# Optimization experiments

Measured on AMD Instinct MI355X. Metric: run time of the kernel, lower is better.

The kernel has to match this reference:

```python
import jax, jax.numpy as jnp
import numpy as np

N_NODES = 50000
N_EDGES = 400000
HIDDEN = 128
OUT_DIM = 1
N_LAYERS = 3
NUM_GRAPHS = 64
VOCAB = 101


def _lin(x, w, b):
    return x @ w + b


def setup_inputs() -> dict:
    key = jax.random.key(0)
    ks = jax.random.split(key, 20)
    inp = {}
    inp['z'] = jax.random.randint(ks[0], (N_NODES,), 0, VOCAB)
    inp['edge_index'] = jax.random.randint(ks[1], (2, N_EDGES), 0, N_NODES)
    inp['edge_attr'] = jax.random.normal(ks[2], (N_EDGES, 1), dtype=jnp.float32)
    inp['batch'] = jnp.sort(jax.random.randint(ks[3], (N_NODES,), 0, NUM_GRAPHS))
    s = 0.05
    inp['embed'] = jax.random.normal(ks[4], (VOCAB, HIDDEN), dtype=jnp.float32) * s
    # per-layer stacked params; weights stored [in, out]
    inp['msg_w1'] = jax.random.normal(ks[5], (N_LAYERS, 2 * HIDDEN + 1, HIDDEN), dtype=jnp.float32) * s
    inp['msg_b1'] = jnp.zeros((N_LAYERS, HIDDEN), dtype=jnp.float32)
    inp['msg_w2'] = jax.random.normal(ks[6], (N_LAYERS, HIDDEN, HIDDEN), dtype=jnp.float32) * s
    inp['msg_b2'] = jnp.zeros((N_LAYERS, HIDDEN), dtype=jnp.float32)
    inp['upd_w1'] = jax.random.normal(ks[7], (N_LAYERS, 2 * HIDDEN, HIDDEN), dtype=jnp.float32) * s
    inp['upd_b1'] = jnp.zeros((N_LAYERS, HIDDEN), dtype=jnp.float32)
    inp['upd_w2'] = jax.random.normal(ks[8], (N_LAYERS, HIDDEN, HIDDEN), dtype=jnp.float32) * s
    inp['upd_b2'] = jnp.zeros((N_LAYERS, HIDDEN), dtype=jnp.float32)
    inp['head_w1'] = jax.random.normal(ks[9], (HIDDEN, HIDDEN), dtype=jnp.float32) * s
    inp['head_b1'] = jnp.zeros((HIDDEN,), dtype=jnp.float32)
    inp['head_w2'] = jax.random.normal(ks[10], (HIDDEN, OUT_DIM), dtype=jnp.float32) * s
    inp['head_b2'] = jnp.zeros((OUT_DIM,), dtype=jnp.float32)
    return inp


def reference(z, edge_index, edge_attr, batch, embed, msg_w1, msg_b1, msg_w2, msg_b2,
              upd_w1, upd_b1, upd_w2, upd_b2, head_w1, head_b1, head_w2, head_b2):
    src, dst = edge_index[0], edge_index[1]
    h = embed[z]  # [N, H]
    for l in range(N_LAYERS):
        m_in = jnp.concatenate([h[src], h[dst], edge_attr], axis=1)  # [E, 2H+1]
        msg = _lin(jax.nn.relu(_lin(m_in, msg_w1[l], msg_b1[l])), msg_w2[l], msg_b2[l])
        agg = jax.ops.segment_sum(msg, dst, num_segments=N_NODES)  # [N, H]
        upd_in = jnp.concatenate([h, agg], axis=1)  # [N, 2H]
        h = h + _lin(jax.nn.relu(_lin(upd_in, upd_w1[l], upd_b1[l])), upd_w2[l], upd_b2[l])
    pooled = jax.ops.segment_sum(h, batch, num_segments=NUM_GRAPHS)
    counts = jax.ops.segment_sum(jnp.ones((h.shape[0], 1), h.dtype), batch, num_segments=NUM_GRAPHS)
    pooled = pooled / jnp.maximum(counts, 1.0)
    return _lin(jax.nn.relu(_lin(pooled, head_w1, head_b1)), head_w2, head_b2)
```

## Files before the change

### kernel.cpp

```cpp
#include <hip/hip_runtime.h>

#define N_NODES 50000
#define NPAD 50048
#define N_EDGES 400000
#define HID 128
#define NUM_GRAPHS 64
#define SCAN_B 196
#define ECAP 2048

typedef __bf16 bf16;
typedef bf16 bf16x8 __attribute__((ext_vector_type(8)));
typedef float f32x4 __attribute__((ext_vector_type(4)));

__device__ inline bf16x8 cvt8(const float* p) {
    const float4 a = *(const float4*)p;
    const float4 b = *(const float4*)(p + 4);
    bf16x8 v;
    v[0] = (bf16)a.x; v[1] = (bf16)a.y; v[2] = (bf16)a.z; v[3] = (bf16)a.w;
    v[4] = (bf16)b.x; v[5] = (bf16)b.y; v[6] = (bf16)b.z; v[7] = (bf16)b.w;
    return v;
}

__device__ __forceinline__ void tile_out(const bf16* lds, bf16* g, int n0, int tid) {
    #pragma unroll
    for (int u = 0; u < 4; ++u) {
        const int unit = u * 256 + tid;
        const int row = unit >> 4;
        const int ci = (unit & 15) * 8;
        *(bf16x8*)&g[(size_t)(n0 + row) * HID + ci] =
            *(const bf16x8*)&lds[row * 136 + ci];
    }
}

__global__ void k_hist(const int* __restrict__ edst, int* __restrict__ deg) {
    int e = blockIdx.x * 256 + threadIdx.x;
    if (e < N_EDGES) atomicAdd(&deg[edst[e]], 1);
}

__global__ void k_scan1(const int* __restrict__ deg, int* __restrict__ partial) {
    __shared__ int buf[256];
    int i = blockIdx.x * 256 + threadIdx.x;
    buf[threadIdx.x] = (i < N_NODES) ? deg[i] : 0;
    __syncthreads();
    for (int off = 128; off > 0; off >>= 1) {
        if (threadIdx.x < off) buf[threadIdx.x] += buf[threadIdx.x + off];
        __syncthreads();
    }
    if (threadIdx.x == 0) partial[blockIdx.x] = buf[0];
}

__global__ void k_scan2(int* __restrict__ partial, int* __restrict__ row_ptr) {
    __shared__ int buf[256];
    int v = (threadIdx.x < SCAN_B) ? partial[threadIdx.x] : 0;
    buf[threadIdx.x] = v;
    __syncthreads();
    for (int off = 1; off < 256; off <<= 1) {
        int t = (threadIdx.x >= off) ? buf[threadIdx.x - off] : 0;
        __syncthreads();
        buf[threadIdx.x] += t;
        __syncthreads();
    }
    if (threadIdx.x < SCAN_B) partial[threadIdx.x] = buf[threadIdx.x] - v;
    if (threadIdx.x == 255) row_ptr[N_NODES] = buf[255];
}

__global__ void k_scan3(const int* __restrict__ deg, const int* __restrict__ partial,
                        int* __restrict__ row_ptr, int* __restrict__ cursor) {
    __shared__ int buf[256];
    int i = blockIdx.x * 256 + threadIdx.x;
    int v = (i < N_NODES) ? deg[i] : 0;
    buf[threadIdx.x] = v;
    __syncthreads();
    for (int off = 1; off < 256; off <<= 1) {
        int t = (threadIdx.x >= off) ? buf[threadIdx.x - off] : 0;
        __syncthreads();
        buf[threadIdx.x] += t;
        __syncthreads();
    }
    if (i < N_NODES) {
        int ex = partial[blockIdx.x] + buf[threadIdx.x] - v;
        row_ptr[i] = ex;
        cursor[i] = ex;
    }
}

__global__ void k_scatter(const int* __restrict__ esrc, const int* __restrict__ edst,
                          const float* __restrict__ attr, int* __restrict__ cursor,
                          int* __restrict__ s_src, float* __restrict__ s_attr) {
    int e = blockIdx.x * 256 + threadIdx.x;
    if (e >= N_EDGES) return;
    int p = atomicAdd(&cursor[edst[e]], 1);
    s_src[p] = esrc[e];
    s_attr[p] = attr[e];
}

__global__ void k_wprep(const float* __restrict__ msg_w1, const float* __restrict__ upd_w1,
                        const float* __restrict__ upd_w2,
                        bf16* __restrict__ W1t, bf16* __restrict__ U1t,
                        bf16* __restrict__ U2t) {
    const int l = blockIdx.y;
    const int n = blockIdx.x, k = threadIdx.x;
    const float* w1  = msg_w1 + (size_t)l * 257 * HID;
    const float* uw1 = upd_w1 + (size_t)l * 2 * HID * HID;
    const float* uw2 = upd_w2 + (size_t)l * HID * HID;
    if (n < 256) {
        W1t[(size_t)l * 256 * HID + n * HID + k] =
            (bf16)w1[(size_t)((n & 128) + k) * HID + (n & 127)];
    } else if (n < 384) {
        const int nn = n - 256;
        U1t[(size_t)l * HID * HID + nn * HID + k] = (bf16)uw1[(size_t)k * HID + nn];
    } else {
        const int nn = n - 384;
        U2t[(size_t)l * HID * HID + nn * HID + k] = (bf16)uw2[(size_t)k * HID + nn];
    }
}

__global__ void k_small(const float* __restrict__ msg_w2, const float* __restrict__ upd_w1,
                        const float* __restrict__ msg_b2,
                        bf16* __restrict__ W2Ut, float* __restrict__ b2u) {
    __shared__ float row[HID];
    const int l = blockIdx.y;
    const int k = blockIdx.x, j = threadIdx.x;
    const float* w2  = msg_w2 + (size_t)l * HID * HID;
    const float* uw1 = upd_w1 + (size_t)l * 2 * HID * HID;
    const float* b2  = msg_b2 + (size_t)l * HID;
    const float* src = (k < HID) ? &w2[(size_t)k * HID] : b2;
    row[j] = src[j];
    __syncthreads();
    float acc = 0.f;
    #pragma unroll 8
    for (int m = 0; m < HID; ++m)
        acc = fmaf(row[m], uw1[(size_t)(HID + m) * HID + j], acc);
    if (k < HID) W2Ut[(size_t)l * HID * HID + (size_t)j * HID + k] = (bf16)acc;
    else b2u[l * HID + j] = acc;
}

__launch_bounds__(256, 4)
__global__ void k_embed_pre(const int* __restrict__ z, const float* __restrict__ embed,
                            const bf16* __restrict__ W1t, const float* __restrict__ b1,
                            bf16* __restrict__ h16, bf16* __restrict__ P, bf16* __restrict__ Q) {
    __shared__ bf16 sH[64 * 136];
    __shared__ bf16 sH2[64 * 136];
    const int tid = threadIdx.x;
    const int n0 = blockIdx.x * 64;
    {
        const int r = tid & 63, cg = tid >> 6;
        const int n = n0 + r;
        const bool valid = n < N_NODES;
        const float* src = valid ? &embed[(size_t)z[n] * HID + cg * 32] : embed;
        #pragma unroll
        for (int i = 0; i < 4; ++i) {
            bf16x8 v;
            if (valid) {
                v = cvt8(src + i * 8);
            } else {
                for (int j = 0; j < 8; ++j) v[j] = (bf16)0.f;
            }
            *(bf16x8*)&sH[r * 136 + cg * 32 + i * 8] = v;
        }
    }
    __syncthreads();
    tile_out(sH, h16, n0, tid);

    const int lane = tid & 63, wave = tid >> 6;
    const int lr = lane & 15, kq = (lane >> 4) * 8, rq = (lane >> 4) * 4;
    const int bcol = wave * 64;

    const f32x4 z4 = {0.f, 0.f, 0.f, 0.f};
    f32x4 acc[4][4];
    #pragma unroll
    for (int mi = 0; mi < 4; ++mi)
        #pragma unroll
        for (int ni = 0; ni < 4; ++ni) acc[mi][ni] = z4;

    #pragma unroll
    for (int ks = 0; ks < 4; ++ks) {
        bf16x8 av[4], bv[4];
        #pragma unroll
        for (int mi = 0; mi < 4; ++mi)
            av[mi] = *(const bf16x8*)&sH[(mi * 16 + lr) * 136 + ks * 32 + kq];
        #pragma unroll
        for (int ni = 0; ni < 4; ++ni)
            bv[ni] = *(const bf16x8*)&W1t[(size_t)(bcol + ni * 16 + lr) * HID + ks * 32 + kq];
        #pragma unroll
        for (int mi = 0; mi < 4; ++mi)
            #pragma unroll
            for (int ni = 0; ni < 4; ++ni)
                acc[mi][ni] = __builtin_amdgcn_mfma_f32_16x16x32_bf16(av[mi], bv[ni],
                                                                      acc[mi][ni], 0, 0, 0);
    }
    __syncthreads();

    {
        bf16* sOut = (bcol < 128) ? sH : sH2;
        const int cb = bcol & 127;
        #pragma unroll
        for (int ni = 0; ni < 4; ++ni) {
            const int c = cb + ni * 16 + lr;
            const float bias = (bcol >= 128) ? b1[c] : 0.f;
            #pragma unroll
            for (int mi = 0; mi < 4; ++mi)
                #pragma unroll
                for (int r = 0; r < 4; ++r)
                    sOut[(mi * 16 + rq + r) * 136 + c] = (bf16)(acc[mi][ni][r] + bias);
        }
    }
    __syncthreads();
    tile_out(sH, P, n0, tid);
    tile_out(sH2, Q, n0, tid);
}

template<int DO_PRE>
__launch_bounds__(256, 4)
__global__ void k_layer(bf16* __restrict__ h16,
                        const bf16* __restrict__ P, const bf16* __restrict__ Q,
                        const int* __restrict__ row_ptr, const int* __restrict__ s_src,
                        const float* __restrict__ s_attr, const float* __restrict__ w1last,
                        const bf16* __restrict__ U1t, const bf16* __restrict__ W2Ut,
                        const float* __restrict__ ub1, const float* __restrict__ b2u,
                        const bf16* __restrict__ U2t, const float* __restrict__ ub2,
                        const bf16* __restrict__ W1tn, const float* __restrict__ b1n,
                        bf16* __restrict__ Pn, bf16* __restrict__ Qn,
                        const int* __restrict__ batch, float* __restrict__ pooled) {
    __shared__ bf16 sAgg[64 * 136];
    __shared__ bf16 sT[64 * 136];
    __shared__ float sDeg[64];
    const int tid = threadIdx.x;
    const int n0 = blockIdx.x * 64;

    {
        int*   sEsrc = (int*)sT;
        float* sEatt = (float*)(sT + ECAP * 2);
        const int elo = row_ptr[n0];
        const int ehi = row_ptr[min(n0 + 64, N_NODES)];
        const int ecap = min(ehi - elo, ECAP);
        for (int i = tid; i < ecap; i += 256) {
            sEsrc[i] = s_src[elo + i];
            sEatt[i] = s_attr[elo + i];
        }
        __syncthreads();

        const int grp = tid >> 4, ln = tid & 15, c8 = ln * 8;
        float wl[8];
        #pragma unroll
        for (int j = 0; j < 8; ++j) wl[j] = w1last[c8 + j];
        #pragma unroll
        for (int t = 0; t < 4; ++t) {
            const int row = t * 16 + grp;
            const int n = n0 + row;
            float a8[8];
            #pragma unroll
            for (int j = 0; j < 8; ++j) a8[j] = 0.f;
            if (n < N_NODES) {
                const int lo = row_ptr[n], hi = row_ptr[n + 1];
                if (ln == 0) sDeg[row] = (float)(hi - lo);
                const bf16x8 qv = *(const bf16x8*)&Q[(size_t)n * HID + c8];
                float q8[8];
                #pragma unroll
                for (int j = 0; j < 8; ++j) q8[j] = (float)qv[j];
                const int llo = lo - elo, lhi = hi - elo;
                if (lhi <= ecap) {
                    int e = llo;
                    for (; e + 4 <= lhi; e += 4) {
                        const int s0 = sEsrc[e], s1 = sEsrc[e + 1];
                        const int s2 = sEsrc[e + 2], s3 = sEsrc[e + 3];
                        const float t0 = sEatt[e], t1 = sEatt[e + 1];
                        const float t2 = sEatt[e + 2], t3 = sEatt[e + 3];
                        const bf16x8 p0 = *(const bf16x8*)&P[(size_t)s0 * HID + c8];
                        const bf16x8 p1 = *(const bf16x8*)&P[(size_t)s1 * HID + c8];
                        const bf16x8 p2 = *(const bf16x8*)&P[(size_t)s2 * HID + c8];
                        const bf16x8 p3 = *(const bf16x8*)&P[(size_t)s3 * HID + c8];
                        #pragma unroll
                        for (int j = 0; j < 8; ++j) {
                            a8[j] += fmaxf(fmaf(t0, wl[j], q8[j] + (float)p0[j]), 0.f);
                            a8[j] += fmaxf(fmaf(t1, wl[j], q8[j] + (float)p1[j]), 0.f);
                            a8[j] += fmaxf(fmaf(t2, wl[j], q8[j] + (float)p2[j]), 0.f);
                            a8[j] += fmaxf(fmaf(t3, wl[j], q8[j] + (float)p3[j]), 0.f);
                        }
                    }
                    for (; e < lhi; ++e) {
                        const int s0 = sEsrc[e];
                        const float t0 = sEatt[e];
                        const bf16x8 p0 = *(const bf16x8*)&P[(size_t)s0 * HID + c8];
                        #pragma unroll
                        for (int j = 0; j < 8; ++j)
                            a8[j] += fmaxf(fmaf(t0, wl[j], q8[j] + (float)p0[j]), 0.f);
                    }
                } else {
                    for (int e = lo; e < hi; ++e) {
                        const int s0 = s_src[e];
                        const float t0 = s_attr[e];
                        const bf16x8 p0 = *(const bf16x8*)&P[(size_t)s0 * HID + c8];
                        #pragma unroll
                        for (int j = 0; j < 8; ++j)
                            a8[j] += fmaxf(fmaf(t0, wl[j], q8[j] + (float)p0[j]), 0.f);
                    }
                }
            } else if (ln == 0) {
                sDeg[row] = 0.f;
            }
            bf16x8 o;
            #pragma unroll
            for (int j = 0; j < 8; ++j) o[j] = (bf16)a8[j];
            *(bf16x8*)&sAgg[row * 136 + c8] = o;
        }
    }
    __syncthreads();

    const int lane = tid & 63, wave = tid >> 6;
    const int lr = lane & 15, kq = (lane >> 4) * 8, rq = (lane >> 4) * 4;
    const int nw = wave * 32;
    const f32x4 z4 = {0.f, 0.f, 0.f, 0.f};

    f32x4 acc[4][2];
    #pragma unroll
    for (int mi = 0; mi < 4; ++mi) { acc[mi][0] = z4; acc[mi][1] = z4; }

    #pragma unroll
    for (int ks = 0; ks < 4; ++ks) {
        bf16x8 av[4], bv[2];
        #pragma unroll
        for (int mi = 0; mi < 4; ++mi)
            av[mi] = *(const bf16x8*)&h16[(size_t)(n0 + mi * 16 + lr) * HID + ks * 32 + kq];
        #pragma unroll
        for (int ni = 0; ni < 2; ++ni)
            bv[ni] = *(const bf16x8*)&U1t[(size_t)(nw + ni * 16 + lr) * HID + ks * 32 + kq];
        #pragma unroll
        for (int mi = 0; mi < 4; ++mi)
            #pragma unroll
            for (int ni = 0; ni < 2; ++ni)
                acc[mi][ni] = __builtin_amdgcn_mfma_f32_16x16x32_bf16(av[mi], bv[ni],
                                                                      acc[mi][ni], 0, 0, 0);
    }
    #pragma unroll
    for (int ks = 0; ks < 4; ++ks) {
        bf16x8 av[4], bv[2];
        #pragma unroll
        for (int mi = 0; mi < 4; ++mi)
            av[mi] = *(const bf16x8*)&sAgg[(mi * 16 + lr) * 136 + ks * 32 + kq];
        #pragma unroll
        for (int ni = 0; ni < 2; ++ni)
            bv[ni] = *(const bf16x8*)&W2Ut[(size_t)(nw + ni * 16 + lr) * HID + ks * 32 + kq];
        #pragma unroll
        for (int mi = 0; mi < 4; ++mi)
            #pragma unroll
            for (int ni = 0; ni < 2; ++ni)
                acc[mi][ni] = __builtin_amdgcn_mfma_f32_16x16x32_bf16(av[mi], bv[ni],
                                                                      acc[mi][ni], 0, 0, 0);
    }
    __syncthreads();

    #pragma unroll
    for (int ni = 0; ni < 2; ++ni) {
        const int c = nw + ni * 16 + lr;
        const float bb1 = ub1[c], bb2 = b2u[c];
        #pragma unroll
        for (int mi = 0; mi < 4; ++mi)
            #pragma unroll
            for (int r = 0; r < 4; ++r) {
                const int row = mi * 16 + rq + r;
                float v = acc[mi][ni][r] + bb1 + sDeg[row] * bb2;
                sT[row * 136 + c] = (bf16)fmaxf(v, 0.f);
            }
    }
    __syncthreads();

    f32x4 acc2[4][2];
    #pragma unroll
    for (int mi = 0; mi < 4; ++mi) { acc2[mi][0] = z4; acc2[mi][1] = z4; }
    #pragma unroll
    for (int ks = 0; ks < 4; ++ks) {
        bf16x8 av[4], bv[2];
        #pragma unroll
        for (int mi = 0; mi < 4; ++mi)
            av[mi] = *(const bf16x8*)&sT[(mi * 16 + lr) * 136 + ks * 32 + kq];
        #pragma unroll
        for (int ni = 0; ni < 2; ++ni)
            bv[ni] = *(const bf16x8*)&U2t[(size_t)(nw + ni * 16 + lr) * HID + ks * 32 + kq];
        #pragma unroll
        for (int mi = 0; mi < 4; ++mi)
            #pragma unroll
            for (int ni = 0; ni < 2; ++ni)
                acc2[mi][ni] = __builtin_amdgcn_mfma_f32_16x16x32_bf16(av[mi], bv[ni],
                                                                       acc2[mi][ni], 0, 0, 0);
    }
    __syncthreads();

    #pragma unroll
    for (int ni = 0; ni < 2; ++ni) {
        const int c = nw + ni * 16 + lr;
        const float bb = ub2[c];
        #pragma unroll
        for (int mi = 0; mi < 4; ++mi)
            #pragma unroll
            for (int r = 0; r < 4; ++r) {
                const int row = mi * 16 + rq + r;
                const int gr = n0 + row;
                float nh = 0.f;
                if (gr < N_NODES) {
                    const size_t off = (size_t)gr * HID + c;
                    nh = (float)h16[off] + acc2[mi][ni][r] + bb;
                }
                sT[row * 136 + c] = (bf16)nh;
                if (DO_PRE) sAgg[row * 136 + c] = (bf16)nh;
            }
    }
    __syncthreads();

    if (DO_PRE) {
        tile_out(sT, h16, n0, tid);

        const int bcol = wave * 64;
        f32x4 pacc[4][4];
        #pragma unroll
        for (int mi = 0; mi < 4; ++mi)
            #pragma unroll
            for (int ni = 0; ni < 4; ++ni) pacc[mi][ni] = z4;

        #pragma unroll
        for (int ks = 0; ks < 4; ++ks) {
            bf16x8 av[4], bv[4];
            #pragma unroll
            for (int mi = 0; mi < 4; ++mi)
                av[mi] = *(const bf16x8*)&sAgg[(mi * 16 + lr) * 136 + ks * 32 + kq];
            #pragma unroll
            for (int ni = 0; ni < 4; ++ni)
                bv[ni] = *(const bf16x8*)&W1tn[(size_t)(bcol + ni * 16 + lr) * HID + ks * 32 + kq];
            #pragma unroll
            for (int mi = 0; mi < 4; ++mi)
                #pragma unroll
                for (int ni = 0; ni < 4; ++ni)
                    pacc[mi][ni] = __builtin_amdgcn_mfma_f32_16x16x32_bf16(av[mi], bv[ni],
                                                                           pacc[mi][ni], 0, 0, 0);
        }
        __syncthreads();

        {
            bf16* sOut = (bcol < 128) ? sT : sAgg;
            const int cb = bcol & 127;
            #pragma unroll
            for (int ni = 0; ni < 4; ++ni) {
                const int c = cb + ni * 16 + lr;
                const float bias = (bcol >= 128) ? b1n[c] : 0.f;
                #pragma unroll
                for (int mi = 0; mi < 4; ++mi)
                    #pragma unroll
                    for (int r = 0; r < 4; ++r)
                        sOut[(mi * 16 + rq + r) * 136 + c] = (bf16)(pacc[mi][ni][r] + bias);
            }
        }
        __syncthreads();
        tile_out(sT, Pn, n0, tid);
        tile_out(sAgg, Qn, n0, tid);
    } else {
        const int c = tid & 127;
        const int half = tid >> 7;
        const int rows = min(64, N_NODES - n0);
        const int rbeg = half * 32;
        const int rend = min(rbeg + 32, rows);
        int cur = -1;
        float s = 0.f;
        for (int r = rbeg; r < rend; ++r) {
            const int g = batch[n0 + r];
            const float v = (float)sT[r * 136 + c];
            if (g != cur) {
                if (cur >= 0) atomicAdd(&pooled[cur * HID + c], s);
                cur = g; s = v;
            } else {
                s += v;
            }
        }
        if (cur >= 0) atomicAdd(&pooled[cur * HID + c], s);
    }
}

__device__ inline int lb(const int* a, int n, int v) {
    int lo = 0, hi = n;
    while (lo < hi) { int m = (lo + hi) >> 1; if (a[m] < v) lo = m + 1; else hi = m; }
    return lo;
}

__global__ void k_head(const float* __restrict__ pooled, const int* __restrict__ batch,
                       const float* __restrict__ hw1, const float* __restrict__ hb1,
                       const float* __restrict__ hw2, const float* __restrict__ hb2,
                       float* __restrict__ out) {
    const int g = blockIdx.x;
    const int c = threadIdx.x;
    __shared__ float sp[HID];
    __shared__ float red[HID];
    __shared__ int sb[2];
    if (c == 0) { sb[0] = lb(batch, N_NODES, g); sb[1] = lb(batch, N_NODES, g + 1); }
    __syncthreads();
    const float cnt = fmaxf((float)(sb[1] - sb[0]), 1.f);
    sp[c] = pooled[g * HID + c] / cnt;
    __syncthreads();
    float acc = hb1[c];
    #pragma unroll 8
    for (int k = 0; k < HID; ++k) acc = fmaf(sp[k], hw1[k * HID + c], acc);
    red[c] = fmaxf(acc, 0.f) * hw2[c];
    __syncthreads();
    for (int s = 64; s > 0; s >>= 1) {
        if (c < s) red[c] += red[c + s];
        __syncthreads();
    }
    if (c == 0) out[g] = red[0] + hb2[0];
}

extern "C" void kernel_launch(void* const* d_in, const int* in_sizes, int n_in,
                              void* d_out, int out_size, void* d_ws, size_t ws_size,
                              hipStream_t stream) {
    const int*   z       = (const int*)d_in[0];
    const int*   ei      = (const int*)d_in[1];
    const float* eattr   = (const float*)d_in[2];
    const int*   batch   = (const int*)d_in[3];
    const float* embed   = (const float*)d_in[4];
    const float* msg_w1  = (const float*)d_in[5];
    const float* msg_b1  = (const float*)d_in[6];
    const float* msg_w2  = (const float*)d_in[7];
    const float* msg_b2  = (const float*)d_in[8];
    const float* upd_w1  = (const float*)d_in[9];
    const float* upd_b1  = (const float*)d_in[10];
    const float* upd_w2  = (const float*)d_in[11];
    const float* upd_b2  = (const float*)d_in[12];
    const float* head_w1 = (const float*)d_in[13];
    const float* head_b1 = (const float*)d_in[14];
    const float* head_w2 = (const float*)d_in[15];
    const float* head_b2 = (const float*)d_in[16];
    float* out = (float*)d_out;

    float* pooled = (float*)d_ws;
    float* b2u    = pooled + NUM_GRAPHS * HID;
    float* s_attr = b2u + 3 * HID;
    int* deg_i    = (int*)(s_attr + N_EDGES);
    int* row_ptr  = deg_i + N_NODES;
    int* partial  = row_ptr + N_NODES + 1;
    int* cursor   = partial + 256;
    int* s_src    = cursor + N_NODES;
    bf16* h16     = (bf16*)((((unsigned long long)(s_src + N_EDGES)) + 15ULL) & ~15ULL);
    bf16* P0      = h16 + (size_t)NPAD * HID;
    bf16* Q0      = P0 + (size_t)NPAD * HID;
    bf16* P1      = Q0 + (size_t)NPAD * HID;
    bf16* Q1      = P1 + (size_t)NPAD * HID;
    bf16* W1t     = Q1 + (size_t)NPAD * HID;
    bf16* U1t     = W1t + 3 * 256 * HID;
    bf16* W2Ut    = U1t + 3 * HID * HID;
    bf16* U2t     = W2Ut + 3 * HID * HID;

    const int* esrc = ei;
    const int* edst = ei + N_EDGES;

    hipMemsetAsync(deg_i, 0, N_NODES * sizeof(int), stream);
    hipMemsetAsync(pooled, 0, NUM_GRAPHS * HID * sizeof(float), stream);
    k_hist<<<(N_EDGES + 255) / 256, 256, 0, stream>>>(edst, deg_i);
    k_scan1<<<SCAN_B, 256, 0, stream>>>(deg_i, partial);
    k_scan2<<<1, 256, 0, stream>>>(partial, row_ptr);
    k_scan3<<<SCAN_B, 256, 0, stream>>>(deg_i, partial, row_ptr, cursor);
    k_scatter<<<(N_EDGES + 255) / 256, 256, 0, stream>>>(esrc, edst, eattr, cursor, s_src, s_attr);
    {
        dim3 g1(512, 3);
        k_wprep<<<g1, 128, 0, stream>>>(msg_w1, upd_w1, upd_w2, W1t, U1t, U2t);
        dim3 g2(HID + 1, 3);
        k_small<<<g2, HID, 0, stream>>>(msg_w2, upd_w1, msg_b2, W2Ut, b2u);
    }

    const int nblk = NPAD / 64;
    k_embed_pre<<<nblk, 256, 0, stream>>>(z, embed, W1t, msg_b1, h16, P0, Q0);

    bf16* Pa = P0; bf16* Qa = Q0; bf16* Pb = P1; bf16* Qb = Q1;
    for (int l = 0; l < 3; ++l) {
        const float* w1last = msg_w1 + (size_t)l * 257 * HID + 256 * HID;
        const bf16* U1l  = U1t  + (size_t)l * HID * HID;
        const bf16* W2Ul = W2Ut + (size_t)l * HID * HID;
        const bf16* U2l  = U2t  + (size_t)l * HID * HID;
        if (l < 2) {
            k_layer<1><<<nblk, 256, 0, stream>>>(
                h16, Pa, Qa, row_ptr, s_src, s_attr, w1last,
                U1l, W2Ul, upd_b1 + (size_t)l * HID, b2u + l * HID,
                U2l, upd_b2 + (size_t)l * HID,
                W1t + (size_t)(l + 1) * 256 * HID, msg_b1 + (size_t)(l + 1) * HID, Pb, Qb,
                nullptr, nullptr);
            bf16* tp = Pa; Pa = Pb; Pb = tp;
            bf16* tq = Qa; Qa = Qb; Qb = tq;
        } else {
            k_layer<0><<<nblk, 256, 0, stream>>>(
                h16, Pa, Qa, row_ptr, s_src, s_attr, w1last,
                U1l, W2Ul, upd_b1 + (size_t)l * HID, b2u + l * HID,
                U2l, upd_b2 + (size_t)l * HID,
                nullptr, nullptr, nullptr, nullptr,
                batch, pooled);
        }
    }
    k_head<<<NUM_GRAPHS, 128, 0, stream>>>(pooled, batch, head_w1, head_b1, head_w2, head_b2, out);
}
```

Before: 277.2 us.

## Split edge aggregation out of fused layer kernel into separate high-occupancy kernel

Moves the per-node gather-and-ReLU edge aggregation out of the fused layer kernel into its own kernel, k_agg. k_agg has a smaller LDS footprint and launch bounds that allow more waves per CU, which should hide the latency of the irregular gathers better. The aggregated result now makes a round trip through a global bf16 buffer, adding an extra write and read of N×128 per layer plus an extra launch. The layer kernel reads the aggregate straight from global memory into its MFMA operands and gets node degrees from a small shared copy of row_ptr.

```diff
diff --git a/kernel.cpp b/kernel.cpp
--- a/kernel.cpp
+++ b/kernel.cpp
@@ -6,7 +6,7 @@
 #define HID 128
 #define NUM_GRAPHS 64
 #define SCAN_B 196
-#define ECAP 2048
+#define EC 1024
 
 typedef __bf16 bf16;
 typedef bf16 bf16x8 __attribute__((ext_vector_type(8)));
@@ -210,102 +210,105 @@
     tile_out(sH2, Q, n0, tid);
 }
 
+__launch_bounds__(256, 6)
+__global__ void k_agg(const bf16* __restrict__ P, const bf16* __restrict__ Q,
+                      const int* __restrict__ row_ptr, const int* __restrict__ s_src,
+                      const float* __restrict__ s_attr, const float* __restrict__ w1last,
+                      bf16* __restrict__ aggH) {
+    __shared__ int   sEsrc[EC];
+    __shared__ float sEatt[EC];
+    const int tid = threadIdx.x;
+    const int n0 = blockIdx.x * 64;
+    const int elo = row_ptr[n0];
+    const int ehi = row_ptr[min(n0 + 64, N_NODES)];
+    const int ecap = min(ehi - elo, EC);
+    for (int i = tid; i < ecap; i += 256) {
+        sEsrc[i] = s_src[elo + i];
+        sEatt[i] = s_attr[elo + i];
+    }
+    __syncthreads();
+
+    const int grp = tid >> 4, ln = tid & 15, c8 = ln * 8;
+    float wl[8];
+    #pragma unroll
+    for (int j = 0; j < 8; ++j) wl[j] = w1last[c8 + j];
+    #pragma unroll
+    for (int t = 0; t < 4; ++t) {
+        const int n = n0 + t * 16 + grp;
+        if (n >= N_NODES) continue;
+        float a8[8];
+        #pragma unroll
+        for (int j = 0; j < 8; ++j) a8[j] = 0.f;
+        const int lo = row_ptr[n], hi = row_ptr[n + 1];
+        const bf16x8 qv = *(const bf16x8*)&Q[(size_t)n * HID + c8];
+        float q8[8];
+        #pragma unroll
+        for (int j = 0; j < 8; ++j) q8[j] = (float)qv[j];
+        const int llo = lo - elo, lhi = hi - elo;
+        if (lhi <= ecap) {
+            int e = llo;
+            for (; e + 4 <= lhi; e += 4) {
+                const int s0 = sEsrc[e], s1 = sEsrc[e + 1];
+                const int s2 = sEsrc[e + 2], s3 = sEsrc[e + 3];
+                const float t0 = sEatt[e], t1 = sEatt[e + 1];
+                const float t2 = sEatt[e + 2], t3 = sEatt[e + 3];
+                const bf16x8 p0 = *(const bf16x8*)&P[(size_t)s0 * HID + c8];
+                const bf16x8 p1 = *(const bf16x8*)&P[(size_t)s1 * HID + c8];
+                const bf16x8 p2 = *(const bf16x8*)&P[(size_t)s2 * HID + c8];
+                const bf16x8 p3 = *(const bf16x8*)&P[(size_t)s3 * HID + c8];
+                #pragma unroll
+                for (int j = 0; j < 8; ++j) {
+                    a8[j] += fmaxf(fmaf(t0, wl[j], q8[j] + (float)p0[j]), 0.f);
+                    a8[j] += fmaxf(fmaf(t1, wl[j], q8[j] + (float)p1[j]), 0.f);
+                    a8[j] += fmaxf(fmaf(t2, wl[j], q8[j] + (float)p2[j]), 0.f);
+                    a8[j] += fmaxf(fmaf(t3, wl[j], q8[j] + (float)p3[j]), 0.f);
+                }
+            }
+            for (; e < lhi; ++e) {
+                const int s0 = sEsrc[e];
+                const float t0 = sEatt[e];
+                const bf16x8 p0 = *(const bf16x8*)&P[(size_t)s0 * HID + c8];
+                #pragma unroll
+                for (int j = 0; j < 8; ++j)
+                    a8[j] += fmaxf(fmaf(t0, wl[j], q8[j] + (float)p0[j]), 0.f);
+            }
+        } else {
+            for (int e = lo; e < hi; ++e) {
+                const int s0 = s_src[e];
+                const float t0 = s_attr[e];
+                const bf16x8 p0 = *(const bf16x8*)&P[(size_t)s0 * HID + c8];
+                #pragma unroll
+                for (int j = 0; j < 8; ++j)
+                    a8[j] += fmaxf(fmaf(t0, wl[j], q8[j] + (float)p0[j]), 0.f);
+            }
+        }
+        bf16x8 o;
+        #pragma unroll
+        for (int j = 0; j < 8; ++j) o[j] = (bf16)a8[j];
+        *(bf16x8*)&aggH[(size_t)n * HID + c8] = o;
+    }
+}
+
 template<int DO_PRE>
 __launch_bounds__(256, 4)
-__global__ void k_layer(bf16* __restrict__ h16,
-                        const bf16* __restrict__ P, const bf16* __restrict__ Q,
-                        const int* __restrict__ row_ptr, const int* __restrict__ s_src,
-                        const float* __restrict__ s_attr, const float* __restrict__ w1last,
+__global__ void k_layer(bf16* __restrict__ h16, const bf16* __restrict__ aggH,
+                        const int* __restrict__ row_ptr,
                         const bf16* __restrict__ U1t, const bf16* __restrict__ W2Ut,
                         const float* __restrict__ ub1, const float* __restrict__ b2u,
                         const bf16* __restrict__ U2t, const float* __restrict__ ub2,
                         const bf16* __restrict__ W1tn, const float* __restrict__ b1n,
                         bf16* __restrict__ Pn, bf16* __restrict__ Qn,
                         const int* __restrict__ batch, float* __restrict__ pooled) {
-    __shared__ bf16 sAgg[64 * 136];
+    __shared__ bf16 sP[64 * 136];
     __shared__ bf16 sT[64 * 136];
     __shared__ float sDeg[64];
+    __shared__ int sRP[65];
     const int tid = threadIdx.x;
     const int n0 = blockIdx.x * 64;
 
-    {
-        int*   sEsrc = (int*)sT;
-        float* sEatt = (float*)(sT + ECAP * 2);
-        const int elo = row_ptr[n0];
-        const int ehi = row_ptr[min(n0 + 64, N_NODES)];
-        const int ecap = min(ehi - elo, ECAP);
-        for (int i = tid; i < ecap; i += 256) {
-            sEsrc[i] = s_src[elo + i];
-            sEatt[i] = s_attr[elo + i];
-        }
-        __syncthreads();
-
-        const int grp = tid >> 4, ln = tid & 15, c8 = ln * 8;
-        float wl[8];
-        #pragma unroll
-        for (int j = 0; j < 8; ++j) wl[j] = w1last[c8 + j];
-        #pragma unroll
-        for (int t = 0; t < 4; ++t) {
-            const int row = t * 16 + grp;
-            const int n = n0 + row;
-            float a8[8];
-            #pragma unroll
-            for (int j = 0; j < 8; ++j) a8[j] = 0.f;
-            if (n < N_NODES) {
-                const int lo = row_ptr[n], hi = row_ptr[n + 1];
-                if (ln == 0) sDeg[row] = (float)(hi - lo);
-                const bf16x8 qv = *(const bf16x8*)&Q[(size_t)n * HID + c8];
-                float q8[8];
-                #pragma unroll
-                for (int j = 0; j < 8; ++j) q8[j] = (float)qv[j];
-                const int llo = lo - elo, lhi = hi - elo;
-                if (lhi <= ecap) {
-                    int e = llo;
-                    for (; e + 4 <= lhi; e += 4) {
-                        const int s0 = sEsrc[e], s1 = sEsrc[e + 1];
-                        const int s2 = sEsrc[e + 2], s3 = sEsrc[e + 3];
-                        const float t0 = sEatt[e], t1 = sEatt[e + 1];
-                        const float t2 = sEatt[e + 2], t3 = sEatt[e + 3];
-                        const bf16x8 p0 = *(const bf16x8*)&P[(size_t)s0 * HID + c8];
-                        const bf16x8 p1 = *(const bf16x8*)&P[(size_t)s1 * HID + c8];
-                        const bf16x8 p2 = *(const bf16x8*)&P[(size_t)s2 * HID + c8];
-                        const bf16x8 p3 = *(const bf16x8*)&P[(size_t)s3 * HID + c8];
-                        #pragma unroll
-                        for (int j = 0; j < 8; ++j) {
-                            a8[j] += fmaxf(fmaf(t0, wl[j], q8[j] + (float)p0[j]), 0.f);
-                            a8[j] += fmaxf(fmaf(t1, wl[j], q8[j] + (float)p1[j]), 0.f);
-                            a8[j] += fmaxf(fmaf(t2, wl[j], q8[j] + (float)p2[j]), 0.f);
-                            a8[j] += fmaxf(fmaf(t3, wl[j], q8[j] + (float)p3[j]), 0.f);
-                        }
-                    }
-                    for (; e < lhi; ++e) {
-                        const int s0 = sEsrc[e];
-                        const float t0 = sEatt[e];
-                        const bf16x8 p0 = *(const bf16x8*)&P[(size_t)s0 * HID + c8];
-                        #pragma unroll
-                        for (int j = 0; j < 8; ++j)
-                            a8[j] += fmaxf(fmaf(t0, wl[j], q8[j] + (float)p0[j]), 0.f);
-                    }
-                } else {
-                    for (int e = lo; e < hi; ++e) {
-                        const int s0 = s_src[e];
-                        const float t0 = s_attr[e];
-                        const bf16x8 p0 = *(const bf16x8*)&P[(size_t)s0 * HID + c8];
-                        #pragma unroll
-                        for (int j = 0; j < 8; ++j)
-                            a8[j] += fmaxf(fmaf(t0, wl[j], q8[j] + (float)p0[j]), 0.f);
-                    }
-                }
-            } else if (ln == 0) {
-                sDeg[row] = 0.f;
-            }
-            bf16x8 o;
-            #pragma unroll
-            for (int j = 0; j < 8; ++j) o[j] = (bf16)a8[j];
-            *(bf16x8*)&sAgg[row * 136 + c8] = o;
-        }
-    }
-    __syncthreads();
+    if (tid < 65) sRP[tid] = row_ptr[min(n0 + tid, N_NODES)];
+    __syncthreads();
+    if (tid < 64) sDeg[tid] = (float)(sRP[tid + 1] - sRP[tid]);
 
     const int lane = tid & 63, wave = tid >> 6;
     const int lr = lane & 15, kq = (lane >> 4) * 8, rq = (lane >> 4) * 4;
@@ -337,7 +340,7 @@
         bf16x8 av[4], bv[2];
         #pragma unroll
         for (int mi = 0; mi < 4; ++mi)
-            av[mi] = *(const bf16x8*)&sAgg[(mi * 16 + lr) * 136 + ks * 32 + kq];
+            av[mi] = *(const bf16x8*)&aggH[(size_t)(n0 + mi * 16 + lr) * HID + ks * 32 + kq];
         #pragma unroll
         for (int ni = 0; ni < 2; ++ni)
             bv[ni] = *(const bf16x8*)&W2Ut[(size_t)(nw + ni * 16 + lr) * HID + ks * 32 + kq];
@@ -395,14 +398,10 @@
             #pragma unroll
             for (int r = 0; r < 4; ++r) {
                 const int row = mi * 16 + rq + r;
-                const int gr = n0 + row;
-                float nh = 0.f;
-                if (gr < N_NODES) {
-                    const size_t off = (size_t)gr * HID + c;
-                    nh = (float)h16[off] + acc2[mi][ni][r] + bb;
-                }
+                const size_t off = (size_t)(n0 + row) * HID + c;
+                const float nh = (float)h16[off] + acc2[mi][ni][r] + bb;
                 sT[row * 136 + c] = (bf16)nh;
-                if (DO_PRE) sAgg[row * 136 + c] = (bf16)nh;
+                if (DO_PRE) sP[row * 136 + c] = (bf16)nh;
             }
     }
     __syncthreads();
@@ -422,7 +421,7 @@
             bf16x8 av[4], bv[4];
             #pragma unroll
             for (int mi = 0; mi < 4; ++mi)
-                av[mi] = *(const bf16x8*)&sAgg[(mi * 16 + lr) * 136 + ks * 32 + kq];
+                av[mi] = *(const bf16x8*)&sP[(mi * 16 + lr) * 136 + ks * 32 + kq];
             #pragma unroll
             for (int ni = 0; ni < 4; ++ni)
                 bv[ni] = *(const bf16x8*)&W1tn[(size_t)(bcol + ni * 16 + lr) * HID + ks * 32 + kq];
@@ -436,7 +435,7 @@
         __syncthreads();
 
         {
-            bf16* sOut = (bcol < 128) ? sT : sAgg;
+            bf16* sOut = (bcol < 128) ? sT : sP;
             const int cb = bcol & 127;
             #pragma unroll
             for (int ni = 0; ni < 4; ++ni) {
@@ -451,7 +450,7 @@
         }
         __syncthreads();
         tile_out(sT, Pn, n0, tid);
-        tile_out(sAgg, Qn, n0, tid);
+        tile_out(sP, Qn, n0, tid);
     } else {
         const int c = tid & 127;
         const int half = tid >> 7;
@@ -537,7 +536,8 @@
     int* cursor   = partial + 256;
     int* s_src    = cursor + N_NODES;
     bf16* h16     = (bf16*)((((unsigned long long)(s_src + N_EDGES)) + 15ULL) & ~15ULL);
-    bf16* P0      = h16 + (size_t)NPAD * HID;
+    bf16* aggH    = h16 + (size_t)NPAD * HID;
+    bf16* P0      = aggH + (size_t)NPAD * HID;
     bf16* Q0      = P0 + (size_t)NPAD * HID;
     bf16* P1      = Q0 + (size_t)NPAD * HID;
     bf16* Q1      = P1 + (size_t)NPAD * HID;
@@ -572,9 +572,10 @@
         const bf16* U1l  = U1t  + (size_t)l * HID * HID;
         const bf16* W2Ul = W2Ut + (size_t)l * HID * HID;
         const bf16* U2l  = U2t  + (size_t)l * HID * HID;
+        k_agg<<<nblk, 256, 0, stream>>>(Pa, Qa, row_ptr, s_src, s_attr, w1last, aggH);
         if (l < 2) {
             k_layer<1><<<nblk, 256, 0, stream>>>(
-                h16, Pa, Qa, row_ptr, s_src, s_attr, w1last,
+                h16, aggH, row_ptr,
                 U1l, W2Ul, upd_b1 + (size_t)l * HID, b2u + l * HID,
                 U2l, upd_b2 + (size_t)l * HID,
                 W1t + (size_t)(l + 1) * 256 * HID, msg_b1 + (size_t)(l + 1) * HID, Pb, Qb,
@@ -583,7 +584,7 @@
             bf16* tq = Qa; Qa = Qb; Qb = tq;
         } else {
             k_layer<0><<<nblk, 256, 0, stream>>>(
-                h16, Pa, Qa, row_ptr, s_src, s_attr, w1last,
+                h16, aggH, row_ptr,
                 U1l, W2Ul, upd_b1 + (size_t)l * HID, b2u + l * HID,
                 U2l, upd_b2 + (size_t)l * HID,
                 nullptr, nullptr, nullptr, nullptr,
```

After: 305.4 us. 10.2% more time.
